# Performance work log

Hardware: AMD Instinct MI355X
Metric: run time of the kernel (lower is better)

The kernel has to match this reference:

```python
import jax, jax.numpy as jnp
import numpy as np

BETA = 0.1
NUM_LAYERS = 2  # GT layers inside each FastGTN


def densify(edge_index, edge_weight, num_nodes):
    # edge_index: [T, 2, E] int, edge_weight: [T, E] -> dense [T, N, N]
    T, _, E = edge_index.shape
    t_ids = jnp.broadcast_to(jnp.arange(T)[:, None], (T, E))
    dense = jnp.zeros((T, num_nodes, num_nodes), dtype=edge_weight.dtype)
    return dense.at[t_ids, edge_index[:, 0, :], edge_index[:, 1, :]].add(edge_weight)


def fast_gtn(dense_A, X, Ws, conv_w, lin_w, lin_b, num_nodes):
    # Ws: [C, w_in, w_out]; conv_w: [L, C, T]; lin_w: [C*w_out, w_out]
    H = jnp.einsum('nk,ckh->cnh', X, Ws)              # [C, N, w_out]
    X_ = jax.lax.stop_gradient(H)                      # clone().detach()
    for l in range(NUM_LAYERS):
        filt = jax.nn.softmax(conv_w[l], axis=1)       # [C, T]
        adj = jnp.einsum('ct,tij->cij', filt, dense_A) # [C, N, N]
        H = jnp.einsum('cij,cjh->cih', adj, H)         # graph conv per channel
    H_ = jax.nn.relu(BETA * X_ + (1.0 - BETA) * H)     # [C, N, w_out]
    H_ = jnp.transpose(H_, (1, 0, 2)).reshape(num_nodes, -1)  # [N, C*w_out]
    return jax.nn.relu(H_ @ lin_w + lin_b)             # [N, w_out]


def setup_inputs() -> dict:
    key = jax.random.key(0)
    ks = jax.random.split(key, 12)
    T, E, N = 4, 131072, 4096
    C, F_IN, H_OUT = 2, 128, 64
    edge_index = jax.random.randint(ks[0], (T, 2, E), 0, N, dtype=jnp.int64)
    edge_weight = jax.random.uniform(ks[1], (T, E), dtype=jnp.float32)
    X = jax.random.normal(ks[2], (N, F_IN), dtype=jnp.float32)
    def glorot(k, shape):
        fan_in, fan_out = shape[-2], shape[-1]
        s = jnp.sqrt(6.0 / (fan_in + fan_out))
        return jax.random.uniform(k, shape, jnp.float32, -s, s)
    # FastGTN #1 (w_in=F_IN)
    Ws1 = glorot(ks[3], (C, F_IN, H_OUT))
    conv_w1 = 0.1 * jax.random.normal(ks[4], (NUM_LAYERS, C, T), dtype=jnp.float32)
    lin_w1 = glorot(ks[5], (C * H_OUT, H_OUT))
    lin_b1 = jnp.zeros((H_OUT,), jnp.float32)
    # FastGTN #2 (w_in=H_OUT)
    Ws2 = glorot(ks[6], (C, H_OUT, H_OUT))
    conv_w2 = 0.1 * jax.random.normal(ks[7], (NUM_LAYERS, C, T), dtype=jnp.float32)
    lin_w2 = glorot(ks[8], (C * H_OUT, H_OUT))
    lin_b2 = jnp.zeros((H_OUT,), jnp.float32)
    return {"edge_index": edge_index, "edge_weight": edge_weight, "X": X,
            "Ws1": Ws1, "conv_w1": conv_w1, "lin_w1": lin_w1, "lin_b1": lin_b1,
            "Ws2": Ws2, "conv_w2": conv_w2, "lin_w2": lin_w2, "lin_b2": lin_b2}


def reference(edge_index, edge_weight, X, Ws1, conv_w1, lin_w1, lin_b1,
              Ws2, conv_w2, lin_w2, lin_b2):
    N = X.shape[0]
    dense_A = densify(edge_index, edge_weight, N)      # [T, N, N]
    H = fast_gtn(dense_A, X, Ws1, conv_w1, lin_w1, lin_b1, N)
    H = fast_gtn(dense_A, H, Ws2, conv_w2, lin_w2, lin_b2, N)
    return H
```

## Files before the change

kernel.cpp:

```cpp
#include <hip/hip_runtime.h>

#define E_EDGES 131072
#define N_NODES 4096
#define HOUT    64
#define NE_TOT  (4 * E_EDGES)
#define CAP     256
#define CSTRIDE 16

__device__ __forceinline__ unsigned short f2bf(float x) {
    unsigned u = __float_as_uint(x);
    return (unsigned short)((u + 0x7FFFu + ((u >> 16) & 1u)) >> 16);
}
__device__ __forceinline__ float bf2f(unsigned b) {
    return __uint_as_float(b << 16);
}

__device__ __forceinline__ void softmax4(const float* __restrict__ cw,
                                         int layer, int c, float f[4]) {
#pragma unroll
    for (int t = 0; t < 4; ++t) f[t] = cw[(layer * 2 + c) * 4 + t];
    float m = fmaxf(fmaxf(f[0], f[1]), fmaxf(f[2], f[3]));
    float s = 0.f;
#pragma unroll
    for (int t = 0; t < 4; ++t) { f[t] = expf(f[t] - m); s += f[t]; }
    float inv = 1.0f / s;
#pragma unroll
    for (int t = 0; t < 4; ++t) f[t] *= inv;
}

__device__ __forceinline__ float selw(const float f[4], int t) {
    float a = (t & 1) ? f[1] : f[0];
    float b = (t & 1) ? f[3] : f[2];
    return (t & 2) ? b : a;
}

__device__ __forceinline__ void fma8(float acc[8], float w, uint4 v) {
    acc[0] += w * bf2f(v.x & 0xFFFFu); acc[1] += w * bf2f(v.x >> 16);
    acc[2] += w * bf2f(v.y & 0xFFFFu); acc[3] += w * bf2f(v.y >> 16);
    acc[4] += w * bf2f(v.z & 0xFFFFu); acc[5] += w * bf2f(v.z >> 16);
    acc[6] += w * bf2f(v.w & 0xFFFFu); acc[7] += w * bf2f(v.w >> 16);
}

__device__ __forceinline__ uint4 pack8(const float acc[8]) {
    uint4 r;
    r.x = (unsigned)f2bf(acc[0]) | ((unsigned)f2bf(acc[1]) << 16);
    r.y = (unsigned)f2bf(acc[2]) | ((unsigned)f2bf(acc[3]) << 16);
    r.z = (unsigned)f2bf(acc[4]) | ((unsigned)f2bf(acc[5]) << 16);
    r.w = (unsigned)f2bf(acc[6]) | ((unsigned)f2bf(acc[7]) << 16);
    return r;
}

__device__ __forceinline__ void spmm_row2c(const uint2* __restrict__ erow, int len,
                                           const unsigned* __restrict__ Hc0,
                                           const unsigned* __restrict__ Hc1,
                                           const float f0[4], const float f1[4],
                                           int lane, float a0[8], float a1[8]) {
    int g  = lane >> 3;
    int hq = lane & 7;
#pragma unroll
    for (int j = 0; j < 8; ++j) { a0[j] = 0.f; a1[j] = 0.f; }
    int e = 0;
    for (; e + 16 <= len; e += 16) {
        uint2 r0 = erow[e + g];
        uint2 r1 = erow[e + 8 + g];
        float w0 = __uint_as_float(r0.y);
        float w1 = __uint_as_float(r1.y);
        int   d0 = r0.x & 0xFFFFu, t0 = (int)(r0.x >> 16);
        int   d1 = r1.x & 0xFFFFu, t1 = (int)(r1.x >> 16);
        uint4 v00 = ((const uint4*)(Hc0 + d0 * (HOUT / 2)))[hq];
        uint4 v01 = ((const uint4*)(Hc1 + d0 * (HOUT / 2)))[hq];
        uint4 v10 = ((const uint4*)(Hc0 + d1 * (HOUT / 2)))[hq];
        uint4 v11 = ((const uint4*)(Hc1 + d1 * (HOUT / 2)))[hq];
        fma8(a0, w0 * selw(f0, t0), v00);
        fma8(a1, w0 * selw(f1, t0), v01);
        fma8(a0, w1 * selw(f0, t1), v10);
        fma8(a1, w1 * selw(f1, t1), v11);
    }
    for (; e + 8 <= len; e += 8) {
        uint2 r0 = erow[e + g];
        float w0 = __uint_as_float(r0.y);
        int   d0 = r0.x & 0xFFFFu, t0 = (int)(r0.x >> 16);
        uint4 v00 = ((const uint4*)(Hc0 + d0 * (HOUT / 2)))[hq];
        uint4 v01 = ((const uint4*)(Hc1 + d0 * (HOUT / 2)))[hq];
        fma8(a0, w0 * selw(f0, t0), v00);
        fma8(a1, w0 * selw(f1, t0), v01);
    }
    if (g < len - e) {
        uint2 r0 = erow[e + g];
        float w0 = __uint_as_float(r0.y);
        int   d0 = r0.x & 0xFFFFu, t0 = (int)(r0.x >> 16);
        uint4 v00 = ((const uint4*)(Hc0 + d0 * (HOUT / 2)))[hq];
        uint4 v01 = ((const uint4*)(Hc1 + d0 * (HOUT / 2)))[hq];
        fma8(a0, w0 * selw(f0, t0), v00);
        fma8(a1, w0 * selw(f1, t0), v01);
    }
#pragma unroll
    for (int j = 0; j < 8; ++j) {
        a0[j] += __shfl_xor(a0[j], 8);
        a0[j] += __shfl_xor(a0[j], 16);
        a0[j] += __shfl_xor(a0[j], 32);
        a1[j] += __shfl_xor(a1[j], 8);
        a1[j] += __shfl_xor(a1[j], 16);
        a1[j] += __shfl_xor(a1[j], 32);
    }
}

__global__ void __launch_bounds__(256)
zero_kernel(int* __restrict__ cursor) {
    cursor[blockIdx.x * 256 + threadIdx.x] = 0;
}

__global__ void __launch_bounds__(256)
zinit_kernel(const float* __restrict__ X, const float* __restrict__ Ws,
             float* __restrict__ H0, unsigned* __restrict__ H016) {
    int idx = blockIdx.x * 256 + threadIdx.x;
    int h = idx & 63;
    int n = (idx >> 6) & (N_NODES - 1);
    int c = idx >> 18;
    const float4* xv = (const float4*)(X + n * 128);
    const float*  w  = Ws + c * 128 * HOUT + h;
    float acc = 0.f;
#pragma unroll 8
    for (int k4 = 0; k4 < 32; ++k4) {
        float4 xx = xv[k4];
        acc += xx.x * w[(k4 * 4 + 0) * HOUT];
        acc += xx.y * w[(k4 * 4 + 1) * HOUT];
        acc += xx.z * w[(k4 * 4 + 2) * HOUT];
        acc += xx.w * w[(k4 * 4 + 3) * HOUT];
    }
    H0[idx] = acc;
    ((unsigned short*)H016)[idx] = f2bf(acc);
}

__global__ void __launch_bounds__(256)
scatter_kernel(const int* __restrict__ ei, const float* __restrict__ ew,
               int* __restrict__ cursor, uint2* __restrict__ edges) {
    int i = blockIdx.x * 256 + threadIdx.x;
    int t = i >> 17;
    int e = i & (E_EDGES - 1);
    int   src = ei[(t * 2 + 0) * E_EDGES + e];
    int   dst = ei[(t * 2 + 1) * E_EDGES + e];
    float w   = ew[t * E_EDGES + e];
    int pos = atomicAdd(&cursor[src * CSTRIDE], 1);
    if (pos < CAP)
        edges[src * CAP + pos] =
            make_uint2((unsigned)dst | ((unsigned)t << 16), __float_as_uint(w));
}

__global__ void __launch_bounds__(256)
spmm_kernel(const int* __restrict__ cnt, const uint2* __restrict__ edges,
            const unsigned* __restrict__ Hin16, unsigned* __restrict__ Hout16,
            const float* __restrict__ cw) {
    int row  = (blockIdx.x * 256 + threadIdx.x) >> 6;
    int lane = threadIdx.x & 63;
    float f0[4], f1[4];
    softmax4(cw, 0, 0, f0);
    softmax4(cw, 0, 1, f1);
    int len = min(cnt[row * CSTRIDE], CAP);
    float a0[8], a1[8];
    spmm_row2c(edges + row * CAP, len,
               Hin16, Hin16 + N_NODES * (HOUT / 2), f0, f1, lane, a0, a1);
    if ((lane >> 3) == 0) {
        int hq = lane & 7;
        ((uint4*)(Hout16 + row * (HOUT / 2)))[hq] = pack8(a0);
        ((uint4*)(Hout16 + (N_NODES + row) * (HOUT / 2)))[hq] = pack8(a1);
    }
}

template <bool FINAL>
__global__ void __launch_bounds__(256)
tail_kernel(const int* __restrict__ cnt, const uint2* __restrict__ edges,
            const unsigned* __restrict__ Hin16,
            const float* __restrict__ H0,
            const float* __restrict__ cw,
            const float* __restrict__ lw, const float* __restrict__ lb,
            const float* __restrict__ Wsn,
            float* __restrict__ outp, unsigned* __restrict__ out16) {
    __shared__ float hcomb[4][2 * HOUT];
    __shared__ float mids[4][HOUT];
    int tid  = threadIdx.x;
    int r    = tid >> 6;
    int lane = tid & 63;
    int row  = blockIdx.x * 4 + r;

    float f0[4], f1[4];
    softmax4(cw, 1, 0, f0);
    softmax4(cw, 1, 1, f1);
    int len = min(cnt[row * CSTRIDE], CAP);
    float a0[8], a1[8];
    spmm_row2c(edges + row * CAP, len,
               Hin16, Hin16 + N_NODES * (HOUT / 2), f0, f1, lane, a0, a1);

    if ((lane >> 3) == 0) {
        int hq = lane & 7;
#pragma unroll
        for (int j = 0; j < 8; ++j) {
            int h = hq * 8 + j;
            float h00 = H0[row * HOUT + h];
            float h01 = H0[(N_NODES + row) * HOUT + h];
            hcomb[r][h]        = fmaxf(0.1f * h00 + 0.9f * a0[j], 0.f);
            hcomb[r][HOUT + h] = fmaxf(0.1f * h01 + 0.9f * a1[j], 0.f);
        }
    }
    __syncthreads();

    float a = lb[lane];
#pragma unroll 8
    for (int j = 0; j < 2 * HOUT; ++j) a += hcomb[r][j] * lw[j * HOUT + lane];

    if (FINAL) {
        outp[row * HOUT + lane] = fmaxf(a, 0.f);
    } else {
        mids[r][lane] = fmaxf(a, 0.f);
        __syncthreads();
#pragma unroll
        for (int c = 0; c < 2; ++c) {
            float acc = 0.f;
            const float* w = Wsn + c * HOUT * HOUT + lane;
#pragma unroll 8
            for (int k = 0; k < HOUT; ++k) acc += mids[r][k] * w[k * HOUT];
            int o = (c * N_NODES + row) * HOUT + lane;
            outp[o] = acc;
            ((unsigned short*)out16)[o] = f2bf(acc);
        }
    }
}

extern "C" void kernel_launch(void* const* d_in, const int* in_sizes, int n_in,
                              void* d_out, int out_size, void* d_ws, size_t ws_size,
                              hipStream_t stream) {
    const int*   ei  = (const int*)d_in[0];
    const float* ew  = (const float*)d_in[1];
    const float* X   = (const float*)d_in[2];
    const float* Ws1 = (const float*)d_in[3];
    const float* cw1 = (const float*)d_in[4];
    const float* lw1 = (const float*)d_in[5];
    const float* lb1 = (const float*)d_in[6];
    const float* Ws2 = (const float*)d_in[7];
    const float* cw2 = (const float*)d_in[8];
    const float* lw2 = (const float*)d_in[9];
    const float* lb2 = (const float*)d_in[10];
    float* outp = (float*)d_out;

    char* ws = (char*)d_ws;
    size_t off = 0;
    auto alloc = [&](size_t bytes) -> void* {
        void* p = ws + off;
        off += (bytes + 255) & ~size_t(255);
        return p;
    };
    int*      cursor = (int*)alloc((size_t)N_NODES * CSTRIDE * 4);
    uint2*    edges  = (uint2*)alloc((size_t)N_NODES * CAP * 8);
    float*    H0a    = (float*)alloc((size_t)2 * N_NODES * HOUT * 4);
    unsigned* H0a16  = (unsigned*)alloc((size_t)2 * N_NODES * HOUT * 2);
    unsigned* Ha16   = (unsigned*)alloc((size_t)2 * N_NODES * HOUT * 2);
    float*    H0b    = (float*)alloc((size_t)2 * N_NODES * HOUT * 4);
    unsigned* H0b16  = (unsigned*)alloc((size_t)2 * N_NODES * HOUT * 2);

    zero_kernel   <<<(N_NODES * CSTRIDE) / 256, 256, 0, stream>>>(cursor);
    zinit_kernel  <<<2048, 256, 0, stream>>>(X, Ws1, H0a, H0a16);
    scatter_kernel<<<NE_TOT / 256, 256, 0, stream>>>(ei, ew, cursor, edges);

    spmm_kernel<<<1024, 256, 0, stream>>>(cursor, edges, H0a16, Ha16, cw1);
    tail_kernel<false><<<1024, 256, 0, stream>>>(
        cursor, edges, Ha16, H0a, cw1, lw1, lb1, Ws2, H0b, H0b16);

    spmm_kernel<<<1024, 256, 0, stream>>>(cursor, edges, H0b16, Ha16, cw2);
    tail_kernel<true><<<1024, 256, 0, stream>>>(
        cursor, edges, Ha16, H0b, cw2, lw2, lb2, nullptr, outp, nullptr);
}
```

Baseline: 116.1 us.

## Partition edge buckets per XCD and pack edge records into 32 bits

The scatter kernel reads the hardware XCC id and appends each edge to a per-source, per-XCD bucket, so atomics on a cursor stay within one die's L2 instead of contending across XCDs. Edge records shrink from 8 to 4 bytes by packing the destination (12 bits), the edge type (2 bits) and a bf16 weight. In the SpMM, each 8-lane group walks one XCD bucket sequentially instead of the groups interleaving over one shared list. The cost is bf16 rounding of edge weights, per-bucket caps of 128 that could drop edges if a bucket overflows, and uneven work across lane groups within a wavefront.

Measured after the change: 125.6 us. 1.08x slower.

```diff
diff --git a/kernel.cpp b/kernel.cpp
--- a/kernel.cpp
+++ b/kernel.cpp
@@ -4,8 +4,8 @@
 #define N_NODES 4096
 #define HOUT    64
 #define NE_TOT  (4 * E_EDGES)
-#define CAP     256
-#define CSTRIDE 16
+#define NXCD    8
+#define CAPX    128
 
 __device__ __forceinline__ unsigned short f2bf(float x) {
     unsigned u = __float_as_uint(x);
@@ -50,23 +50,24 @@
     return r;
 }
 
-__device__ __forceinline__ void spmm_row2c(const uint2* __restrict__ erow, int len,
+__device__ __forceinline__ void spmm_row2c(const unsigned* __restrict__ rowe,
+                                           const int* __restrict__ cnt8,
                                            const unsigned* __restrict__ Hc0,
                                            const unsigned* __restrict__ Hc1,
                                            const float f0[4], const float f1[4],
                                            int lane, float a0[8], float a1[8]) {
     int g  = lane >> 3;
     int hq = lane & 7;
+    int len = min(cnt8[g], CAPX);
+    const unsigned* seg = rowe + g * CAPX;
 #pragma unroll
     for (int j = 0; j < 8; ++j) { a0[j] = 0.f; a1[j] = 0.f; }
     int e = 0;
-    for (; e + 16 <= len; e += 16) {
-        uint2 r0 = erow[e + g];
-        uint2 r1 = erow[e + 8 + g];
-        float w0 = __uint_as_float(r0.y);
-        float w1 = __uint_as_float(r1.y);
-        int   d0 = r0.x & 0xFFFFu, t0 = (int)(r0.x >> 16);
-        int   d1 = r1.x & 0xFFFFu, t1 = (int)(r1.x >> 16);
+    for (; e + 2 <= len; e += 2) {
+        unsigned r0 = seg[e], r1 = seg[e + 1];
+        int   d0 = r0 & 0xFFF, t0 = (r0 >> 12) & 3;
+        int   d1 = r1 & 0xFFF, t1 = (r1 >> 12) & 3;
+        float w0 = bf2f(r0 >> 16), w1 = bf2f(r1 >> 16);
         uint4 v00 = ((const uint4*)(Hc0 + d0 * (HOUT / 2)))[hq];
         uint4 v01 = ((const uint4*)(Hc1 + d0 * (HOUT / 2)))[hq];
         uint4 v10 = ((const uint4*)(Hc0 + d1 * (HOUT / 2)))[hq];
@@ -76,19 +77,10 @@
         fma8(a0, w1 * selw(f0, t1), v10);
         fma8(a1, w1 * selw(f1, t1), v11);
     }
-    for (; e + 8 <= len; e += 8) {
-        uint2 r0 = erow[e + g];
-        float w0 = __uint_as_float(r0.y);
-        int   d0 = r0.x & 0xFFFFu, t0 = (int)(r0.x >> 16);
-        uint4 v00 = ((const uint4*)(Hc0 + d0 * (HOUT / 2)))[hq];
-        uint4 v01 = ((const uint4*)(Hc1 + d0 * (HOUT / 2)))[hq];
-        fma8(a0, w0 * selw(f0, t0), v00);
-        fma8(a1, w0 * selw(f1, t0), v01);
-    }
-    if (g < len - e) {
-        uint2 r0 = erow[e + g];
-        float w0 = __uint_as_float(r0.y);
-        int   d0 = r0.x & 0xFFFFu, t0 = (int)(r0.x >> 16);
+    if (e < len) {
+        unsigned r0 = seg[e];
+        int   d0 = r0 & 0xFFF, t0 = (r0 >> 12) & 3;
+        float w0 = bf2f(r0 >> 16);
         uint4 v00 = ((const uint4*)(Hc0 + d0 * (HOUT / 2)))[hq];
         uint4 v01 = ((const uint4*)(Hc1 + d0 * (HOUT / 2)))[hq];
         fma8(a0, w0 * selw(f0, t0), v00);
@@ -134,21 +126,23 @@
 
 __global__ void __launch_bounds__(256)
 scatter_kernel(const int* __restrict__ ei, const float* __restrict__ ew,
-               int* __restrict__ cursor, uint2* __restrict__ edges) {
+               int* __restrict__ cursor, unsigned* __restrict__ edges) {
+    unsigned xcd;
+    asm volatile("s_getreg_b32 %0, hwreg(HW_REG_XCC_ID, 0, 4)" : "=s"(xcd));
     int i = blockIdx.x * 256 + threadIdx.x;
     int t = i >> 17;
     int e = i & (E_EDGES - 1);
     int   src = ei[(t * 2 + 0) * E_EDGES + e];
     int   dst = ei[(t * 2 + 1) * E_EDGES + e];
     float w   = ew[t * E_EDGES + e];
-    int pos = atomicAdd(&cursor[src * CSTRIDE], 1);
-    if (pos < CAP)
-        edges[src * CAP + pos] =
-            make_uint2((unsigned)dst | ((unsigned)t << 16), __float_as_uint(w));
-}
-
-__global__ void __launch_bounds__(256)
-spmm_kernel(const int* __restrict__ cnt, const uint2* __restrict__ edges,
+    unsigned rec = ((unsigned)f2bf(w) << 16) | ((unsigned)t << 12) | (unsigned)dst;
+    int pos = atomicAdd(&cursor[src * NXCD + xcd], 1);
+    if (pos < CAPX)
+        edges[(src * NXCD + xcd) * CAPX + pos] = rec;
+}
+
+__global__ void __launch_bounds__(256)
+spmm_kernel(const int* __restrict__ cnt, const unsigned* __restrict__ edges,
             const unsigned* __restrict__ Hin16, unsigned* __restrict__ Hout16,
             const float* __restrict__ cw) {
     int row  = (blockIdx.x * 256 + threadIdx.x) >> 6;
@@ -156,9 +150,8 @@
     float f0[4], f1[4];
     softmax4(cw, 0, 0, f0);
     softmax4(cw, 0, 1, f1);
-    int len = min(cnt[row * CSTRIDE], CAP);
     float a0[8], a1[8];
-    spmm_row2c(edges + row * CAP, len,
+    spmm_row2c(edges + row * NXCD * CAPX, cnt + row * NXCD,
                Hin16, Hin16 + N_NODES * (HOUT / 2), f0, f1, lane, a0, a1);
     if ((lane >> 3) == 0) {
         int hq = lane & 7;
@@ -169,7 +162,7 @@
 
 template <bool FINAL>
 __global__ void __launch_bounds__(256)
-tail_kernel(const int* __restrict__ cnt, const uint2* __restrict__ edges,
+tail_kernel(const int* __restrict__ cnt, const unsigned* __restrict__ edges,
             const unsigned* __restrict__ Hin16,
             const float* __restrict__ H0,
             const float* __restrict__ cw,
@@ -186,9 +179,8 @@
     float f0[4], f1[4];
     softmax4(cw, 1, 0, f0);
     softmax4(cw, 1, 1, f1);
-    int len = min(cnt[row * CSTRIDE], CAP);
     float a0[8], a1[8];
-    spmm_row2c(edges + row * CAP, len,
+    spmm_row2c(edges + row * NXCD * CAPX, cnt + row * NXCD,
                Hin16, Hin16 + N_NODES * (HOUT / 2), f0, f1, lane, a0, a1);
 
     if ((lane >> 3) == 0) {
@@ -249,15 +241,15 @@
         off += (bytes + 255) & ~size_t(255);
         return p;
     };
-    int*      cursor = (int*)alloc((size_t)N_NODES * CSTRIDE * 4);
-    uint2*    edges  = (uint2*)alloc((size_t)N_NODES * CAP * 8);
+    int*      cursor = (int*)alloc((size_t)N_NODES * NXCD * 4);
+    unsigned* edges  = (unsigned*)alloc((size_t)N_NODES * NXCD * CAPX * 4);
     float*    H0a    = (float*)alloc((size_t)2 * N_NODES * HOUT * 4);
     unsigned* H0a16  = (unsigned*)alloc((size_t)2 * N_NODES * HOUT * 2);
     unsigned* Ha16   = (unsigned*)alloc((size_t)2 * N_NODES * HOUT * 2);
     float*    H0b    = (float*)alloc((size_t)2 * N_NODES * HOUT * 4);
     unsigned* H0b16  = (unsigned*)alloc((size_t)2 * N_NODES * HOUT * 2);
 
-    zero_kernel   <<<(N_NODES * CSTRIDE) / 256, 256, 0, stream>>>(cursor);
+    zero_kernel   <<<(N_NODES * NXCD) / 256, 256, 0, stream>>>(cursor);
     zinit_kernel  <<<2048, 256, 0, stream>>>(X, Ws1, H0a, H0a16);
     scatter_kernel<<<NE_TOT / 256, 256, 0, stream>>>(ei, ew, cursor, edges);
 
```

## Pack edge records into 32 bits with bf16 weights and fold cursor zeroing

Applied to the files above, without the earlier changes.

Edge records shrink from 8 bytes to 4 by packing a 12-bit destination, a 2-bit type and a bf16 weight into one word. This halves edge-list traffic in the scatter and all four SpMM passes. Cursor zeroing moves into the zinit kernel, removing one launch, and the scatter uses nontemporal loads and stores. Rounding edge weights to bf16 adds numerical error, and the packing assumes N fits in 12 bits.

After: 119.3 us. +2.8%, slower.

```diff
diff --git a/kernel.cpp b/kernel.cpp
--- a/kernel.cpp
+++ b/kernel.cpp
@@ -50,7 +50,7 @@
     return r;
 }
 
-__device__ __forceinline__ void spmm_row2c(const uint2* __restrict__ erow, int len,
+__device__ __forceinline__ void spmm_row2c(const unsigned* __restrict__ rowe, int len,
                                            const unsigned* __restrict__ Hc0,
                                            const unsigned* __restrict__ Hc1,
                                            const float f0[4], const float f1[4],
@@ -61,12 +61,11 @@
     for (int j = 0; j < 8; ++j) { a0[j] = 0.f; a1[j] = 0.f; }
     int e = 0;
     for (; e + 16 <= len; e += 16) {
-        uint2 r0 = erow[e + g];
-        uint2 r1 = erow[e + 8 + g];
-        float w0 = __uint_as_float(r0.y);
-        float w1 = __uint_as_float(r1.y);
-        int   d0 = r0.x & 0xFFFFu, t0 = (int)(r0.x >> 16);
-        int   d1 = r1.x & 0xFFFFu, t1 = (int)(r1.x >> 16);
+        unsigned r0 = rowe[e + g];
+        unsigned r1 = rowe[e + 8 + g];
+        int   d0 = r0 & 0xFFF, t0 = (r0 >> 12) & 3;
+        int   d1 = r1 & 0xFFF, t1 = (r1 >> 12) & 3;
+        float w0 = bf2f(r0 >> 16), w1 = bf2f(r1 >> 16);
         uint4 v00 = ((const uint4*)(Hc0 + d0 * (HOUT / 2)))[hq];
         uint4 v01 = ((const uint4*)(Hc1 + d0 * (HOUT / 2)))[hq];
         uint4 v10 = ((const uint4*)(Hc0 + d1 * (HOUT / 2)))[hq];
@@ -77,18 +76,18 @@
         fma8(a1, w1 * selw(f1, t1), v11);
     }
     for (; e + 8 <= len; e += 8) {
-        uint2 r0 = erow[e + g];
-        float w0 = __uint_as_float(r0.y);
-        int   d0 = r0.x & 0xFFFFu, t0 = (int)(r0.x >> 16);
+        unsigned r0 = rowe[e + g];
+        int   d0 = r0 & 0xFFF, t0 = (r0 >> 12) & 3;
+        float w0 = bf2f(r0 >> 16);
         uint4 v00 = ((const uint4*)(Hc0 + d0 * (HOUT / 2)))[hq];
         uint4 v01 = ((const uint4*)(Hc1 + d0 * (HOUT / 2)))[hq];
         fma8(a0, w0 * selw(f0, t0), v00);
         fma8(a1, w0 * selw(f1, t0), v01);
     }
     if (g < len - e) {
-        uint2 r0 = erow[e + g];
-        float w0 = __uint_as_float(r0.y);
-        int   d0 = r0.x & 0xFFFFu, t0 = (int)(r0.x >> 16);
+        unsigned r0 = rowe[e + g];
+        int   d0 = r0 & 0xFFF, t0 = (r0 >> 12) & 3;
+        float w0 = bf2f(r0 >> 16);
         uint4 v00 = ((const uint4*)(Hc0 + d0 * (HOUT / 2)))[hq];
         uint4 v01 = ((const uint4*)(Hc1 + d0 * (HOUT / 2)))[hq];
         fma8(a0, w0 * selw(f0, t0), v00);
@@ -106,14 +105,11 @@
 }
 
 __global__ void __launch_bounds__(256)
-zero_kernel(int* __restrict__ cursor) {
-    cursor[blockIdx.x * 256 + threadIdx.x] = 0;
-}
-
-__global__ void __launch_bounds__(256)
 zinit_kernel(const float* __restrict__ X, const float* __restrict__ Ws,
-             float* __restrict__ H0, unsigned* __restrict__ H016) {
+             float* __restrict__ H0, unsigned* __restrict__ H016,
+             int* __restrict__ cursor) {
     int idx = blockIdx.x * 256 + threadIdx.x;
+    if (idx < N_NODES * CSTRIDE) cursor[idx] = 0;
     int h = idx & 63;
     int n = (idx >> 6) & (N_NODES - 1);
     int c = idx >> 18;
@@ -134,21 +130,21 @@
 
 __global__ void __launch_bounds__(256)
 scatter_kernel(const int* __restrict__ ei, const float* __restrict__ ew,
-               int* __restrict__ cursor, uint2* __restrict__ edges) {
+               int* __restrict__ cursor, unsigned* __restrict__ edges) {
     int i = blockIdx.x * 256 + threadIdx.x;
     int t = i >> 17;
     int e = i & (E_EDGES - 1);
-    int   src = ei[(t * 2 + 0) * E_EDGES + e];
-    int   dst = ei[(t * 2 + 1) * E_EDGES + e];
-    float w   = ew[t * E_EDGES + e];
+    int   src = __builtin_nontemporal_load(ei + (t * 2 + 0) * E_EDGES + e);
+    int   dst = __builtin_nontemporal_load(ei + (t * 2 + 1) * E_EDGES + e);
+    float w   = __builtin_nontemporal_load(ew + t * E_EDGES + e);
+    unsigned rec = ((unsigned)f2bf(w) << 16) | ((unsigned)t << 12) | (unsigned)dst;
     int pos = atomicAdd(&cursor[src * CSTRIDE], 1);
     if (pos < CAP)
-        edges[src * CAP + pos] =
-            make_uint2((unsigned)dst | ((unsigned)t << 16), __float_as_uint(w));
-}
-
-__global__ void __launch_bounds__(256)
-spmm_kernel(const int* __restrict__ cnt, const uint2* __restrict__ edges,
+        __builtin_nontemporal_store(rec, &edges[src * CAP + pos]);
+}
+
+__global__ void __launch_bounds__(256)
+spmm_kernel(const int* __restrict__ cnt, const unsigned* __restrict__ edges,
             const unsigned* __restrict__ Hin16, unsigned* __restrict__ Hout16,
             const float* __restrict__ cw) {
     int row  = (blockIdx.x * 256 + threadIdx.x) >> 6;
@@ -169,7 +165,7 @@
 
 template <bool FINAL>
 __global__ void __launch_bounds__(256)
-tail_kernel(const int* __restrict__ cnt, const uint2* __restrict__ edges,
+tail_kernel(const int* __restrict__ cnt, const unsigned* __restrict__ edges,
             const unsigned* __restrict__ Hin16,
             const float* __restrict__ H0,
             const float* __restrict__ cw,
@@ -250,15 +246,14 @@
         return p;
     };
     int*      cursor = (int*)alloc((size_t)N_NODES * CSTRIDE * 4);
-    uint2*    edges  = (uint2*)alloc((size_t)N_NODES * CAP * 8);
+    unsigned* edges  = (unsigned*)alloc((size_t)N_NODES * CAP * 4);
     float*    H0a    = (float*)alloc((size_t)2 * N_NODES * HOUT * 4);
     unsigned* H0a16  = (unsigned*)alloc((size_t)2 * N_NODES * HOUT * 2);
     unsigned* Ha16   = (unsigned*)alloc((size_t)2 * N_NODES * HOUT * 2);
     float*    H0b    = (float*)alloc((size_t)2 * N_NODES * HOUT * 4);
     unsigned* H0b16  = (unsigned*)alloc((size_t)2 * N_NODES * HOUT * 2);
 
-    zero_kernel   <<<(N_NODES * CSTRIDE) / 256, 256, 0, stream>>>(cursor);
-    zinit_kernel  <<<2048, 256, 0, stream>>>(X, Ws1, H0a, H0a16);
+    zinit_kernel  <<<2048, 256, 0, stream>>>(X, Ws1, H0a, H0a16, cursor);
     scatter_kernel<<<NE_TOT / 256, 256, 0, stream>>>(ei, ew, cursor, edges);
 
     spmm_kernel<<<1024, 256, 0, stream>>>(cursor, edges, H0a16, Ha16, cw1);
```
